# Kernel optimization log

Measured on AMD Instinct MI355X. Metric: run time of the kernel, lower is better.

The kernel has to match this reference:

```python
import jax, jax.numpy as jnp
import numpy as np

N_NODES = 100000
N_EDGES = 1600000
D = 64


def setup_inputs() -> dict:
    key = jax.random.key(0)
    k1, k2, k3, k4, k5, k6, k7, k8 = jax.random.split(key, 8)
    x = jax.random.normal(k1, (N_NODES, D), dtype=jnp.float32)
    adj = jax.random.randint(k2, (2, N_EDGES), 0, N_NODES, dtype=jnp.int64)
    adj_wts = jax.random.uniform(k3, (N_EDGES,), dtype=jnp.float32)
    s = 1.0 / np.sqrt(D)
    W1 = jax.random.uniform(k4, (D, D), minval=-s, maxval=s, dtype=jnp.float32)
    b1 = jax.random.uniform(k5, (D,), minval=-s, maxval=s, dtype=jnp.float32)
    W2 = jax.random.uniform(k6, (D, D), minval=-s, maxval=s, dtype=jnp.float32)
    b2 = jax.random.uniform(k7, (D,), minval=-s, maxval=s, dtype=jnp.float32)
    return {"x": x, "adj": adj, "adj_wts": adj_wts,
            "W1": W1, "b1": b1, "W2": W2, "b2": b2}


def _gcn_conv(x, row, col, norm, W, b):
    # Linear transform first (PyG GCNConv order), then normalized aggregation.
    h = x @ W                                   # [N, D]
    msg = norm[:, None] * h[row]                # gather from source nodes [E+N, D]
    out = jax.ops.segment_sum(msg, col, num_segments=N_NODES)  # scatter to targets
    return out + b


def _gcn_norm(adj, adj_wts):
    # Add self-loops with weight 1, compute symmetric normalization.
    loop = jnp.arange(N_NODES, dtype=adj.dtype)
    row = jnp.concatenate([adj[0], loop])
    col = jnp.concatenate([adj[1], loop])
    w = jnp.concatenate([adj_wts, jnp.ones((N_NODES,), dtype=adj_wts.dtype)])
    deg = jax.ops.segment_sum(w, col, num_segments=N_NODES)
    dinv = jnp.where(deg > 0, jax.lax.rsqrt(jnp.maximum(deg, 1e-12)), 0.0)
    norm = dinv[row] * w * dinv[col]
    return row, col, norm


def reference(x, adj, adj_wts, W1, b1, W2, b2):
    row, col, norm = _gcn_norm(adj, adj_wts)
    h = jax.nn.relu(_gcn_conv(x, row, col, norm, W1, b1))
    h = jax.nn.relu(_gcn_conv(h, row, col, norm, W2, b2))
    return h
```

## Files before the change

kernel.cpp:

```cpp
#include <hip/hip_runtime.h>

#define N_NODES 100000
#define N_EDGES 1600000
#define D 64
#define NBUCK 391
#define GBE 391
#define EPB 4096
#define DCAP 6144
#define NTILES 6250

typedef __attribute__((ext_vector_type(8))) short bf16x8;
typedef __attribute__((ext_vector_type(4))) float f32x4;

__device__ __forceinline__ unsigned short f2bf(float f) {
    unsigned int i = __float_as_uint(f);
    i += 0x7FFFu + ((i >> 16) & 1u);
    return (unsigned short)(i >> 16);
}
__device__ __forceinline__ void fma8(float* a, uint4 v, float wv) {
    a[0] = fmaf(wv, __uint_as_float(v.x << 16), a[0]);
    a[1] = fmaf(wv, __uint_as_float(v.x & 0xFFFF0000u), a[1]);
    a[2] = fmaf(wv, __uint_as_float(v.y << 16), a[2]);
    a[3] = fmaf(wv, __uint_as_float(v.y & 0xFFFF0000u), a[3]);
    a[4] = fmaf(wv, __uint_as_float(v.z << 16), a[4]);
    a[5] = fmaf(wv, __uint_as_float(v.z & 0xFFFF0000u), a[5]);
    a[6] = fmaf(wv, __uint_as_float(v.w << 16), a[6]);
    a[7] = fmaf(wv, __uint_as_float(v.w & 0xFFFF0000u), a[7]);
}


__global__ void binA(const int* __restrict__ col, int* __restrict__ histT) {
    __shared__ int h[NBUCK];
    int t = threadIdx.x;
    for (int i = t; i < NBUCK; i += 256) h[i] = 0;
    __syncthreads();
    int e0 = blockIdx.x * EPB;
    for (int i = t; i < EPB; i += 256) {
        int e = e0 + i;
        if (e < N_EDGES) atomicAdd(&h[col[e] >> 8], 1);
    }
    __syncthreads();
    for (int i = t; i < NBUCK; i += 256) histT[i * GBE + blockIdx.x] = h[i];
}

__global__ void binB1(int* __restrict__ histT, int* __restrict__ rowtot) {
    __shared__ int s[512];
    int b = blockIdx.x, tid = threadIdx.x;
    int v = (tid < GBE) ? histT[b * GBE + tid] : 0;
    s[tid] = v;
    __syncthreads();
    for (int o = 1; o < 512; o <<= 1) {
        int t = (tid >= o) ? s[tid - o] : 0;
        __syncthreads();
        s[tid] += t;
        __syncthreads();
    }
    if (tid < GBE) histT[b * GBE + tid] = s[tid] - v;
    if (tid == 511) rowtot[b] = s[511];
}

__global__ void binB2(const int* __restrict__ rowtot, int* __restrict__ bucketOff) {
    __shared__ int s[512];
    int tid = threadIdx.x;
    int v = (tid < NBUCK) ? rowtot[tid] : 0;
    s[tid] = v;
    __syncthreads();
    for (int o = 1; o < 512; o <<= 1) {
        int t = (tid >= o) ? s[tid - o] : 0;
        __syncthreads();
        s[tid] += t;
        __syncthreads();
    }
    if (tid < NBUCK) bucketOff[tid] = s[tid] - v;
    if (tid == 0) bucketOff[NBUCK] = N_EDGES;
}

__global__ void binC(const int* __restrict__ row, const int* __restrict__ col,
                     const float* __restrict__ w, const int* __restrict__ histT,
                     const int* __restrict__ bucketOff, int2* __restrict__ part_sw,
                     unsigned char* __restrict__ part_dlo) {
    __shared__ int cur[NBUCK];
    int t = threadIdx.x;
    for (int i = t; i < NBUCK; i += 256)
        cur[i] = bucketOff[i] + histT[i * GBE + blockIdx.x];
    __syncthreads();
    int e0 = blockIdx.x * EPB;
    for (int i = t; i < EPB; i += 256) {
        int e = e0 + i;
        if (e >= N_EDGES) continue;
        int c = col[e];
        int pos = atomicAdd(&cur[c >> 8], 1);
        int2 p; p.x = row[e]; p.y = __float_as_int(w[e]);
        part_sw[pos] = p;
        part_dlo[pos] = (unsigned char)(c & 255);
    }
}

__global__ void binD(const int2* __restrict__ part_sw, const unsigned char* __restrict__ part_dlo,
                     const int* __restrict__ bucketOff, int2* __restrict__ epack,
                     int* __restrict__ base, float* __restrict__ dinv) {
    __shared__ unsigned short dlo[DCAP];
    __shared__ int hist[257];
    __shared__ int cur[256];
    __shared__ float wsum[256];
    int b = blockIdx.x, t = threadIdx.x;
    int s0 = bucketOff[b], m = bucketOff[b + 1] - s0;
    for (int i = t; i < 257; i += 256) hist[i] = 0;
    wsum[t] = 0.0f;
    __syncthreads();
    for (int i = t; i < m; i += 256) {
        int dl = part_dlo[s0 + i];
        dlo[i] = (unsigned short)dl;
        atomicAdd(&hist[dl], 1);
    }
    __syncthreads();
    if (t == 0) {
        int acc = 0;
        for (int i = 0; i < 256; ++i) { int v = hist[i]; hist[i] = acc; acc += v; }
        hist[256] = acc;
    }
    __syncthreads();
    cur[t] = hist[t];
    int dst = b * 256 + t;
    if (dst < N_NODES) base[dst] = s0 + hist[t];
    if (b == NBUCK - 1 && t == 0) base[N_NODES] = N_EDGES;
    __syncthreads();
    for (int i = t; i < m; i += 256) {
        int dl = dlo[i];
        int2 p = part_sw[s0 + i];
        int pos = s0 + atomicAdd(&cur[dl], 1);
        epack[pos] = p;
        atomicAdd(&wsum[dl], __int_as_float(p.y));
    }
    __syncthreads();
    if (dst < N_NODES) dinv[dst] = rsqrtf(1.0f + wsum[t]);
}

__global__ void prescale_bf16(const float4* __restrict__ in4, const float* __restrict__ dinv,
                              ushort4* __restrict__ out4) {
    int gid = blockIdx.x * 256 + threadIdx.x;
    if (gid >= N_NODES * (D / 4)) return;
    float s = dinv[gid >> 4];
    float4 v = in4[gid];
    ushort4 o;
    o.x = f2bf(s * v.x); o.y = f2bf(s * v.y);
    o.z = f2bf(s * v.z); o.w = f2bf(s * v.w);
    out4[gid] = o;
}

template <bool LAST>
__global__ __launch_bounds__(256, 4)
void gcn_layer(const unsigned short* __restrict__ xsb, const float* __restrict__ W,
               const float* __restrict__ b, const float* __restrict__ dinv,
               const int2* __restrict__ epack, const int* __restrict__ base,
               unsigned short* __restrict__ hb_out, float* __restrict__ f_out) {
    __shared__ unsigned short T[16 * 72];
    int t = threadIdx.x;
    int lane  = t & 63;
    int wid   = t >> 6;
    int g     = lane >> 3;
    int c8    = (lane & 7) * 8;
    int r16   = lane & 15;
    int halfk = (lane >> 4) * 8;

    int bcol = wid * 16 + r16;
    bf16x8 bf0, bf1;
#pragma unroll
    for (int i = 0; i < 8; ++i) bf0[i] = (short)f2bf(W[(halfk + i) * D + bcol]);
#pragma unroll
    for (int i = 0; i < 8; ++i) bf1[i] = (short)f2bf(W[(halfk + 32 + i) * D + bcol]);
    float bias = b[bcol];

    int node0 = blockIdx.x * 16;
    for (int jp = 0; jp < 2; ++jp) {
        int nA = node0 + wid * 4 + jp * 2;
        int nB = nA + 1;
        float aA[8], aB[8];
#pragma unroll
        for (int q = 0; q < 8; ++q) { aA[q] = 0.0f; aB[q] = 0.0f; }
        if (g == 0) {
            uint4 sv = *(const uint4*)(xsb + (size_t)nA * D + c8);
            fma8(aA, sv, 1.0f);
        }
        if (g == 1) {
            uint4 sv = *(const uint4*)(xsb + (size_t)nB * D + c8);
            fma8(aB, sv, 1.0f);
        }
        int kA = base[nA], enA = base[nA + 1];
        int kB = enA,      enB = base[nB + 1];
        while (kA < enA || kB < enB) {
            uint4 vA, vB;
            float wA = 0.0f, wB = 0.0f;
            bool doA = kA < enA, doB = kB < enB;
            if (doA) {
                int kg = kA + g;
                int kc = (kg < enA) ? kg : (enA - 1);
                int2 p = epack[kc];
                wA = (kg < enA) ? __int_as_float(p.y) : 0.0f;
                vA = *(const uint4*)(xsb + (size_t)p.x * D + c8);
            }
            if (doB) {
                int kg = kB + g;
                int kc = (kg < enB) ? kg : (enB - 1);
                int2 p = epack[kc];
                wB = (kg < enB) ? __int_as_float(p.y) : 0.0f;
                vB = *(const uint4*)(xsb + (size_t)p.x * D + c8);
            }
            if (doA) fma8(aA, vA, wA);
            if (doB) fma8(aB, vB, wB);
            kA += 8; kB += 8;
        }
#pragma unroll
        for (int q = 0; q < 8; ++q) {
            aA[q] += __shfl_xor(aA[q], 8);
            aB[q] += __shfl_xor(aB[q], 8);
            aA[q] += __shfl_xor(aA[q], 16);
            aB[q] += __shfl_xor(aB[q], 16);
            aA[q] += __shfl_xor(aA[q], 32);
            aB[q] += __shfl_xor(aB[q], 32);
        }
        if (lane < 16) {
            float* a = (lane < 8) ? aA : aB;
            int nl = wid * 4 + jp * 2 + (lane >> 3);
            int l8 = (lane & 7) * 8;
            uint4 pk;
            pk.x = ((unsigned)f2bf(a[1]) << 16) | f2bf(a[0]);
            pk.y = ((unsigned)f2bf(a[3]) << 16) | f2bf(a[2]);
            pk.z = ((unsigned)f2bf(a[5]) << 16) | f2bf(a[4]);
            pk.w = ((unsigned)f2bf(a[7]) << 16) | f2bf(a[6]);
            *(uint4*)&T[nl * 72 + l8] = pk;
        }
    }
    __syncthreads();
    bf16x8 af0 = *(const bf16x8*)&T[r16 * 72 + halfk];
    bf16x8 af1 = *(const bf16x8*)&T[r16 * 72 + halfk + 32];
    f32x4 acc = {0.f, 0.f, 0.f, 0.f};
    acc = __builtin_amdgcn_mfma_f32_16x16x32_bf16(af0, bf0, acc, 0, 0, 0);
    acc = __builtin_amdgcn_mfma_f32_16x16x32_bf16(af1, bf1, acc, 0, 0, 0);
#pragma unroll
    for (int i = 0; i < 4; ++i) {
        int nr = (lane >> 4) * 4 + i;
        int node = node0 + nr;
        float s = dinv[node];
        float y = fmaxf(fmaf(s, acc[i], bias), 0.0f);
        size_t oidx = (size_t)node * D + bcol;
        if (LAST) f_out[oidx] = y;
        else      hb_out[oidx] = f2bf(s * y);
    }
}

extern "C" void kernel_launch(void* const* d_in, const int* in_sizes, int n_in,
                              void* d_out, int out_size, void* d_ws, size_t ws_size,
                              hipStream_t stream) {
    const float* x       = (const float*)d_in[0];
    const int*   adj     = (const int*)d_in[1];
    const float* adj_wts = (const float*)d_in[2];
    const float* W1      = (const float*)d_in[3];
    const float* b1      = (const float*)d_in[4];
    const float* W2      = (const float*)d_in[5];
    const float* b2      = (const float*)d_in[6];
    float* out = (float*)d_out;

    const int* row = adj;
    const int* col = adj + N_EDGES;

    char* p = (char*)d_ws;
    int2* epack = (int2*)p;                   p += (size_t)N_EDGES * 8;
    unsigned short* xsb = (unsigned short*)p; p += (size_t)N_NODES * D * 2;
    unsigned short* hb  = (unsigned short*)p; p += (size_t)N_NODES * D * 2;
    int2* part_sw = (int2*)p;                 p += (size_t)N_EDGES * 8;
    unsigned char* part_dlo = (unsigned char*)p; p += N_EDGES;
    int* histT = (int*)p;                     p += (size_t)(NBUCK * GBE + 3) / 4 * 4 * 4;
    int* rowtot = (int*)p;                    p += 392 * 4;
    int* bucketOff = (int*)p;                 p += 392 * 4;
    int* base = (int*)p;                      p += 100004 * 4;
    float* dinv = (float*)p;                  p += 100000 * 4;

    const int nblk_c = (N_NODES * 16 + 255) / 256;

    binA<<<GBE, 256, 0, stream>>>(col, histT);
    binB1<<<NBUCK, 512, 0, stream>>>(histT, rowtot);
    binB2<<<1, 512, 0, stream>>>(rowtot, bucketOff);
    binC<<<GBE, 256, 0, stream>>>(row, col, adj_wts, histT, bucketOff, part_sw, part_dlo);
    binD<<<NBUCK, 256, 0, stream>>>(part_sw, part_dlo, bucketOff, epack, base, dinv);

    prescale_bf16<<<nblk_c, 256, 0, stream>>>((const float4*)x, dinv, (ushort4*)xsb);

    gcn_layer<false><<<NTILES, 256, 0, stream>>>(xsb, W1, b1, dinv, epack, base, hb, nullptr);
    gcn_layer<true ><<<NTILES, 256, 0, stream>>>(hb, W2, b2, dinv, epack, base, nullptr, out);
}
```

Before: 198.8 us.

## Fuse bf16 prescale into binD and gather four nodes per wave concurrently

The separate prescale kernel is folded into the tail of binD, so each bucket block scales and converts its 256 nodes of x to bf16 right after computing dinv, which removes one launch and a dinv reload. The aggregation loop in gcn_layer now walks four destination nodes at once per wave instead of two nodes over two passes, putting more independent gathers in flight to hide memory latency. The cost is more registers (four 8-float accumulators), which could lower occupancy under the launch bounds, and the loop now runs until the longest of four neighbor lists is done, so more lanes sit idle when degrees differ.

```diff
diff --git a/kernel.cpp b/kernel.cpp
--- a/kernel.cpp
+++ b/kernel.cpp
@@ -27,6 +27,14 @@
     a[6] = fmaf(wv, __uint_as_float(v.w << 16), a[6]);
     a[7] = fmaf(wv, __uint_as_float(v.w & 0xFFFF0000u), a[7]);
 }
+__device__ __forceinline__ void packrow(unsigned short* dst, const float* a) {
+    uint4 pk;
+    pk.x = ((unsigned)f2bf(a[1]) << 16) | f2bf(a[0]);
+    pk.y = ((unsigned)f2bf(a[3]) << 16) | f2bf(a[2]);
+    pk.z = ((unsigned)f2bf(a[5]) << 16) | f2bf(a[4]);
+    pk.w = ((unsigned)f2bf(a[7]) << 16) | f2bf(a[6]);
+    *(uint4*)dst = pk;
+}
 
 
 __global__ void binA(const int* __restrict__ col, int* __restrict__ histT) {
@@ -97,8 +105,9 @@
 }
 
 __global__ void binD(const int2* __restrict__ part_sw, const unsigned char* __restrict__ part_dlo,
-                     const int* __restrict__ bucketOff, int2* __restrict__ epack,
-                     int* __restrict__ base, float* __restrict__ dinv) {
+                     const int* __restrict__ bucketOff, const float4* __restrict__ x4,
+                     int2* __restrict__ epack, int* __restrict__ base,
+                     float* __restrict__ dinv, ushort4* __restrict__ xsb4) {
     __shared__ unsigned short dlo[DCAP];
     __shared__ int hist[257];
     __shared__ int cur[256];
@@ -133,19 +142,28 @@
         atomicAdd(&wsum[dl], __int_as_float(p.y));
     }
     __syncthreads();
-    if (dst < N_NODES) dinv[dst] = rsqrtf(1.0f + wsum[t]);
-}
-
-__global__ void prescale_bf16(const float4* __restrict__ in4, const float* __restrict__ dinv,
-                              ushort4* __restrict__ out4) {
-    int gid = blockIdx.x * 256 + threadIdx.x;
-    if (gid >= N_NODES * (D / 4)) return;
-    float s = dinv[gid >> 4];
-    float4 v = in4[gid];
-    ushort4 o;
-    o.x = f2bf(s * v.x); o.y = f2bf(s * v.y);
-    o.z = f2bf(s * v.z); o.w = f2bf(s * v.w);
-    out4[gid] = o;
+    float di = 0.0f;
+    if (dst < N_NODES) {
+        di = rsqrtf(1.0f + wsum[t]);
+        dinv[dst] = di;
+    }
+    wsum[t] = di;
+    __syncthreads();
+    int nvalid = N_NODES - b * 256;
+#pragma unroll
+    for (int i = 0; i < 16; ++i) {
+        int gid = t + i * 256;
+        int r = gid >> 4, ch = gid & 15;
+        if (r < nvalid) {
+            float s = wsum[r];
+            size_t fidx = (size_t)(b * 256 + r) * 16 + ch;
+            float4 v = x4[fidx];
+            ushort4 o;
+            o.x = f2bf(s * v.x); o.y = f2bf(s * v.y);
+            o.z = f2bf(s * v.z); o.w = f2bf(s * v.w);
+            xsb4[fidx] = o;
+        }
+    }
 }
 
 template <bool LAST>
@@ -172,64 +190,60 @@
     float bias = b[bcol];
 
     int node0 = blockIdx.x * 16;
-    for (int jp = 0; jp < 2; ++jp) {
-        int nA = node0 + wid * 4 + jp * 2;
-        int nB = nA + 1;
-        float aA[8], aB[8];
-#pragma unroll
-        for (int q = 0; q < 8; ++q) { aA[q] = 0.0f; aB[q] = 0.0f; }
-        if (g == 0) {
-            uint4 sv = *(const uint4*)(xsb + (size_t)nA * D + c8);
-            fma8(aA, sv, 1.0f);
-        }
-        if (g == 1) {
-            uint4 sv = *(const uint4*)(xsb + (size_t)nB * D + c8);
-            fma8(aB, sv, 1.0f);
-        }
-        int kA = base[nA], enA = base[nA + 1];
-        int kB = enA,      enB = base[nB + 1];
-        while (kA < enA || kB < enB) {
-            uint4 vA, vB;
-            float wA = 0.0f, wB = 0.0f;
-            bool doA = kA < enA, doB = kB < enB;
-            if (doA) {
-                int kg = kA + g;
-                int kc = (kg < enA) ? kg : (enA - 1);
-                int2 p = epack[kc];
-                wA = (kg < enA) ? __int_as_float(p.y) : 0.0f;
-                vA = *(const uint4*)(xsb + (size_t)p.x * D + c8);
-            }
-            if (doB) {
-                int kg = kB + g;
-                int kc = (kg < enB) ? kg : (enB - 1);
-                int2 p = epack[kc];
-                wB = (kg < enB) ? __int_as_float(p.y) : 0.0f;
-                vB = *(const uint4*)(xsb + (size_t)p.x * D + c8);
-            }
-            if (doA) fma8(aA, vA, wA);
-            if (doB) fma8(aB, vB, wB);
-            kA += 8; kB += 8;
-        }
-#pragma unroll
-        for (int q = 0; q < 8; ++q) {
-            aA[q] += __shfl_xor(aA[q], 8);
-            aB[q] += __shfl_xor(aB[q], 8);
-            aA[q] += __shfl_xor(aA[q], 16);
-            aB[q] += __shfl_xor(aB[q], 16);
-            aA[q] += __shfl_xor(aA[q], 32);
-            aB[q] += __shfl_xor(aB[q], 32);
-        }
-        if (lane < 16) {
-            float* a = (lane < 8) ? aA : aB;
-            int nl = wid * 4 + jp * 2 + (lane >> 3);
-            int l8 = (lane & 7) * 8;
-            uint4 pk;
-            pk.x = ((unsigned)f2bf(a[1]) << 16) | f2bf(a[0]);
-            pk.y = ((unsigned)f2bf(a[3]) << 16) | f2bf(a[2]);
-            pk.z = ((unsigned)f2bf(a[5]) << 16) | f2bf(a[4]);
-            pk.w = ((unsigned)f2bf(a[7]) << 16) | f2bf(a[6]);
-            *(uint4*)&T[nl * 72 + l8] = pk;
-        }
+    int n0 = node0 + wid * 4;
+
+    float a0[8], a1[8], a2[8], a3[8];
+#pragma unroll
+    for (int q = 0; q < 8; ++q) { a0[q] = 0.f; a1[q] = 0.f; a2[q] = 0.f; a3[q] = 0.f; }
+
+    if (g == 0)      { uint4 sv = *(const uint4*)(xsb + (size_t)(n0    ) * D + c8); fma8(a0, sv, 1.0f); }
+    else if (g == 1) { uint4 sv = *(const uint4*)(xsb + (size_t)(n0 + 1) * D + c8); fma8(a1, sv, 1.0f); }
+    else if (g == 2) { uint4 sv = *(const uint4*)(xsb + (size_t)(n0 + 2) * D + c8); fma8(a2, sv, 1.0f); }
+    else if (g == 3) { uint4 sv = *(const uint4*)(xsb + (size_t)(n0 + 3) * D + c8); fma8(a3, sv, 1.0f); }
+
+    int k0 = base[n0],     e0 = base[n0 + 1];
+    int k1 = e0,           e1 = base[n0 + 2];
+    int k2 = e1,           e2 = base[n0 + 3];
+    int k3 = e2,           e3 = base[n0 + 4];
+
+    while (k0 < e0 || k1 < e1 || k2 < e2 || k3 < e3) {
+        uint4 v0, v1, v2, v3;
+        float w0 = 0.f, w1 = 0.f, w2 = 0.f, w3 = 0.f;
+        bool d0 = k0 < e0, d1 = k1 < e1, d2 = k2 < e2, d3 = k3 < e3;
+        if (d0) { int kg = k0 + g; int kc = (kg < e0) ? kg : e0 - 1; int2 p = epack[kc];
+                  w0 = (kg < e0) ? __int_as_float(p.y) : 0.f;
+                  v0 = *(const uint4*)(xsb + (size_t)p.x * D + c8); }
+        if (d1) { int kg = k1 + g; int kc = (kg < e1) ? kg : e1 - 1; int2 p = epack[kc];
+                  w1 = (kg < e1) ? __int_as_float(p.y) : 0.f;
+                  v1 = *(const uint4*)(xsb + (size_t)p.x * D + c8); }
+        if (d2) { int kg = k2 + g; int kc = (kg < e2) ? kg : e2 - 1; int2 p = epack[kc];
+                  w2 = (kg < e2) ? __int_as_float(p.y) : 0.f;
+                  v2 = *(const uint4*)(xsb + (size_t)p.x * D + c8); }
+        if (d3) { int kg = k3 + g; int kc = (kg < e3) ? kg : e3 - 1; int2 p = epack[kc];
+                  w3 = (kg < e3) ? __int_as_float(p.y) : 0.f;
+                  v3 = *(const uint4*)(xsb + (size_t)p.x * D + c8); }
+        if (d0) fma8(a0, v0, w0);
+        if (d1) fma8(a1, v1, w1);
+        if (d2) fma8(a2, v2, w2);
+        if (d3) fma8(a3, v3, w3);
+        k0 += 8; k1 += 8; k2 += 8; k3 += 8;
+    }
+
+#pragma unroll
+    for (int q = 0; q < 8; ++q) {
+        a0[q] += __shfl_xor(a0[q], 8);  a1[q] += __shfl_xor(a1[q], 8);
+        a2[q] += __shfl_xor(a2[q], 8);  a3[q] += __shfl_xor(a3[q], 8);
+        a0[q] += __shfl_xor(a0[q], 16); a1[q] += __shfl_xor(a1[q], 16);
+        a2[q] += __shfl_xor(a2[q], 16); a3[q] += __shfl_xor(a3[q], 16);
+        a0[q] += __shfl_xor(a0[q], 32); a1[q] += __shfl_xor(a1[q], 32);
+        a2[q] += __shfl_xor(a2[q], 32); a3[q] += __shfl_xor(a3[q], 32);
+    }
+    {
+        int l8 = (lane & 7) * 8;
+        if (g == 0)      packrow(&T[(wid * 4 + 0) * 72 + l8], a0);
+        else if (g == 1) packrow(&T[(wid * 4 + 1) * 72 + l8], a1);
+        else if (g == 2) packrow(&T[(wid * 4 + 2) * 72 + l8], a2);
+        else if (g == 3) packrow(&T[(wid * 4 + 3) * 72 + l8], a3);
     }
     __syncthreads();
     bf16x8 af0 = *(const bf16x8*)&T[r16 * 72 + halfk];
@@ -276,15 +290,12 @@
     int* base = (int*)p;                      p += 100004 * 4;
     float* dinv = (float*)p;                  p += 100000 * 4;
 
-    const int nblk_c = (N_NODES * 16 + 255) / 256;
-
     binA<<<GBE, 256, 0, stream>>>(col, histT);
     binB1<<<NBUCK, 512, 0, stream>>>(histT, rowtot);
     binB2<<<1, 512, 0, stream>>>(rowtot, bucketOff);
     binC<<<GBE, 256, 0, stream>>>(row, col, adj_wts, histT, bucketOff, part_sw, part_dlo);
-    binD<<<NBUCK, 256, 0, stream>>>(part_sw, part_dlo, bucketOff, epack, base, dinv);
-
-    prescale_bf16<<<nblk_c, 256, 0, stream>>>((const float4*)x, dinv, (ushort4*)xsb);
+    binD<<<NBUCK, 256, 0, stream>>>(part_sw, part_dlo, bucketOff, (const float4*)x,
+                                    epack, base, dinv, (ushort4*)xsb);
 
     gcn_layer<false><<<NTILES, 256, 0, stream>>>(xsb, W1, b1, dinv, epack, base, hb, nullptr);
     gcn_layer<true ><<<NTILES, 256, 0, stream>>>(hb, W2, b2, dinv, epack, base, nullptr, out);
```

Result: slower. 234.6 us (+18.0%).

## Fuse binning scans and prescale, pack dst-low bits into source index

Applied to the files above, without the earlier changes.

Merges the two scan kernels into one using a last-block-done atomic counter, packs the low 8 destination bits into the top byte of the source index to drop the separate byte array, and folds the bf16 prescale of x into binD. It also replaces binD's serial single-thread scan with a parallel scan and removes clamped loads in the edge gather loop. Together these cut kernel launches and global traffic in the preprocessing chain, at the cost of an extra memset and a grid-level atomic handshake.

```diff
diff --git a/kernel.cpp b/kernel.cpp
--- a/kernel.cpp
+++ b/kernel.cpp
@@ -43,8 +43,10 @@
     for (int i = t; i < NBUCK; i += 256) histT[i * GBE + blockIdx.x] = h[i];
 }
 
-__global__ void binB1(int* __restrict__ histT, int* __restrict__ rowtot) {
+__global__ void binB(int* __restrict__ histT, int* __restrict__ rowtot,
+                     int* __restrict__ bucketOff, int* __restrict__ done) {
     __shared__ int s[512];
+    __shared__ int lastflag;
     int b = blockIdx.x, tid = threadIdx.x;
     int v = (tid < GBE) ? histT[b * GBE + tid] : 0;
     s[tid] = v;
@@ -56,29 +58,31 @@
         __syncthreads();
     }
     if (tid < GBE) histT[b * GBE + tid] = s[tid] - v;
-    if (tid == 511) rowtot[b] = s[511];
-}
-
-__global__ void binB2(const int* __restrict__ rowtot, int* __restrict__ bucketOff) {
-    __shared__ int s[512];
-    int tid = threadIdx.x;
-    int v = (tid < NBUCK) ? rowtot[tid] : 0;
-    s[tid] = v;
-    __syncthreads();
-    for (int o = 1; o < 512; o <<= 1) {
-        int t = (tid >= o) ? s[tid - o] : 0;
-        __syncthreads();
-        s[tid] += t;
-        __syncthreads();
-    }
-    if (tid < NBUCK) bucketOff[tid] = s[tid] - v;
-    if (tid == 0) bucketOff[NBUCK] = N_EDGES;
+    if (tid == 511) atomicExch(&rowtot[b], s[511]);
+    __syncthreads();
+    if (tid == 0) {
+        __threadfence();
+        lastflag = (atomicAdd(done, 1) == NBUCK - 1);
+    }
+    __syncthreads();
+    if (lastflag) {
+        int rv = (tid < NBUCK) ? atomicAdd(&rowtot[tid], 0) : 0;
+        s[tid] = rv;
+        __syncthreads();
+        for (int o = 1; o < 512; o <<= 1) {
+            int t = (tid >= o) ? s[tid - o] : 0;
+            __syncthreads();
+            s[tid] += t;
+            __syncthreads();
+        }
+        if (tid < NBUCK) bucketOff[tid] = s[tid] - rv;
+        if (tid == 0) bucketOff[NBUCK] = N_EDGES;
+    }
 }
 
 __global__ void binC(const int* __restrict__ row, const int* __restrict__ col,
                      const float* __restrict__ w, const int* __restrict__ histT,
-                     const int* __restrict__ bucketOff, int2* __restrict__ part_sw,
-                     unsigned char* __restrict__ part_dlo) {
+                     const int* __restrict__ bucketOff, int2* __restrict__ part_sw) {
     __shared__ int cur[NBUCK];
     int t = threadIdx.x;
     for (int i = t; i < NBUCK; i += 256)
@@ -90,62 +94,81 @@
         if (e >= N_EDGES) continue;
         int c = col[e];
         int pos = atomicAdd(&cur[c >> 8], 1);
-        int2 p; p.x = row[e]; p.y = __float_as_int(w[e]);
+        int2 p;
+        p.x = (int)((unsigned)row[e] | ((unsigned)(c & 255) << 24));
+        p.y = __float_as_int(w[e]);
         part_sw[pos] = p;
-        part_dlo[pos] = (unsigned char)(c & 255);
-    }
-}
-
-__global__ void binD(const int2* __restrict__ part_sw, const unsigned char* __restrict__ part_dlo,
-                     const int* __restrict__ bucketOff, int2* __restrict__ epack,
-                     int* __restrict__ base, float* __restrict__ dinv) {
+    }
+}
+
+__global__ void binD(const int2* __restrict__ part_sw, const int* __restrict__ bucketOff,
+                     const float4* __restrict__ x4, int2* __restrict__ epack,
+                     int* __restrict__ base, float* __restrict__ dinv,
+                     ushort4* __restrict__ xsb4) {
     __shared__ unsigned short dlo[DCAP];
-    __shared__ int hist[257];
+    __shared__ int hist[256];
+    __shared__ int scanb[256];
     __shared__ int cur[256];
     __shared__ float wsum[256];
     int b = blockIdx.x, t = threadIdx.x;
     int s0 = bucketOff[b], m = bucketOff[b + 1] - s0;
-    for (int i = t; i < 257; i += 256) hist[i] = 0;
+    hist[t] = 0;
     wsum[t] = 0.0f;
     __syncthreads();
     for (int i = t; i < m; i += 256) {
-        int dl = part_dlo[s0 + i];
+        int dl = (int)((unsigned)part_sw[s0 + i].x >> 24);
         dlo[i] = (unsigned short)dl;
         atomicAdd(&hist[dl], 1);
     }
     __syncthreads();
-    if (t == 0) {
-        int acc = 0;
-        for (int i = 0; i < 256; ++i) { int v = hist[i]; hist[i] = acc; acc += v; }
-        hist[256] = acc;
-    }
-    __syncthreads();
-    cur[t] = hist[t];
+    int v = hist[t];
+    scanb[t] = v;
+    __syncthreads();
+    for (int o = 1; o < 256; o <<= 1) {
+        int tv = (t >= o) ? scanb[t - o] : 0;
+        __syncthreads();
+        scanb[t] += tv;
+        __syncthreads();
+    }
+    int excl = scanb[t] - v;
+    cur[t] = excl;
     int dst = b * 256 + t;
-    if (dst < N_NODES) base[dst] = s0 + hist[t];
+    if (dst < N_NODES) base[dst] = s0 + excl;
     if (b == NBUCK - 1 && t == 0) base[N_NODES] = N_EDGES;
     __syncthreads();
     for (int i = t; i < m; i += 256) {
         int dl = dlo[i];
         int2 p = part_sw[s0 + i];
         int pos = s0 + atomicAdd(&cur[dl], 1);
-        epack[pos] = p;
+        int2 q;
+        q.x = (int)((unsigned)p.x & 0xFFFFFFu);
+        q.y = p.y;
+        epack[pos] = q;
         atomicAdd(&wsum[dl], __int_as_float(p.y));
     }
     __syncthreads();
-    if (dst < N_NODES) dinv[dst] = rsqrtf(1.0f + wsum[t]);
-}
-
-__global__ void prescale_bf16(const float4* __restrict__ in4, const float* __restrict__ dinv,
-                              ushort4* __restrict__ out4) {
-    int gid = blockIdx.x * 256 + threadIdx.x;
-    if (gid >= N_NODES * (D / 4)) return;
-    float s = dinv[gid >> 4];
-    float4 v = in4[gid];
-    ushort4 o;
-    o.x = f2bf(s * v.x); o.y = f2bf(s * v.y);
-    o.z = f2bf(s * v.z); o.w = f2bf(s * v.w);
-    out4[gid] = o;
+    float di = 0.0f;
+    if (dst < N_NODES) {
+        di = rsqrtf(1.0f + wsum[t]);
+        dinv[dst] = di;
+    }
+    wsum[t] = di;
+    __syncthreads();
+    int nvalid = N_NODES - b * 256;
+#pragma unroll
+    for (int i = 0; i < 16; ++i) {
+        int gid = t + i * 256;
+        int r = gid >> 4, ch = gid & 15;
+        if (r < nvalid) {
+            float s = wsum[r];
+            size_t fidx = (size_t)(b * 256 + r) * 16 + ch;
+            float4 xv = x4[fidx];
+            ushort4 o;
+            o.x = f2bf(s * xv.x); o.y = f2bf(s * xv.y);
+            o.z = f2bf(s * xv.z); o.w = f2bf(s * xv.w);
+            xsb4[fidx] = o;
+        }
+    }
 }
 
 template <bool LAST>
@@ -189,25 +212,16 @@
         int kA = base[nA], enA = base[nA + 1];
         int kB = enA,      enB = base[nB + 1];
         while (kA < enA || kB < enB) {
+            int kgA = kA + g, kgB = kB + g;
+            bool dA = kgA < enA, dB = kgB < enB;
+            int2 pA, pB;
             uint4 vA, vB;
-            float wA = 0.0f, wB = 0.0f;
-            bool doA = kA < enA, doB = kB < enB;
-            if (doA) {
-                int kg = kA + g;
-                int kc = (kg < enA) ? kg : (enA - 1);
-                int2 p = epack[kc];
-                wA = (kg < enA) ? __int_as_float(p.y) : 0.0f;
-                vA = *(const uint4*)(xsb + (size_t)p.x * D + c8);
-            }
-            if (doB) {
-                int kg = kB + g;
-                int kc = (kg < enB) ? kg : (enB - 1);
-                int2 p = epack[kc];
-                wB = (kg < enB) ? __int_as_float(p.y) : 0.0f;
-                vB = *(const uint4*)(xsb + (size_t)p.x * D + c8);
-            }
-            if (doA) fma8(aA, vA, wA);
-            if (doB) fma8(aB, vB, wB);
+            if (dA) pA = epack[kgA];
+            if (dB) pB = epack[kgB];
+            if (dA) vA = *(const uint4*)(xsb + (size_t)pA.x * D + c8);
+            if (dB) vB = *(const uint4*)(xsb + (size_t)pB.x * D + c8);
+            if (dA) fma8(aA, vA, __int_as_float(pA.y));
+            if (dB) fma8(aB, vB, __int_as_float(pB.y));
             kA += 8; kB += 8;
         }
 #pragma unroll
@@ -269,22 +283,19 @@
     unsigned short* xsb = (unsigned short*)p; p += (size_t)N_NODES * D * 2;
     unsigned short* hb  = (unsigned short*)p; p += (size_t)N_NODES * D * 2;
     int2* part_sw = (int2*)p;                 p += (size_t)N_EDGES * 8;
-    unsigned char* part_dlo = (unsigned char*)p; p += N_EDGES;
     int* histT = (int*)p;                     p += (size_t)(NBUCK * GBE + 3) / 4 * 4 * 4;
     int* rowtot = (int*)p;                    p += 392 * 4;
     int* bucketOff = (int*)p;                 p += 392 * 4;
     int* base = (int*)p;                      p += 100004 * 4;
     float* dinv = (float*)p;                  p += 100000 * 4;
-
-    const int nblk_c = (N_NODES * 16 + 255) / 256;
+    int* done = (int*)p;                      p += 4 * 4;
 
     binA<<<GBE, 256, 0, stream>>>(col, histT);
-    binB1<<<NBUCK, 512, 0, stream>>>(histT, rowtot);
-    binB2<<<1, 512, 0, stream>>>(rowtot, bucketOff);
-    binC<<<GBE, 256, 0, stream>>>(row, col, adj_wts, histT, bucketOff, part_sw, part_dlo);
-    binD<<<NBUCK, 256, 0, stream>>>(part_sw, part_dlo, bucketOff, epack, base, dinv);
-
-    prescale_bf16<<<nblk_c, 256, 0, stream>>>((const float4*)x, dinv, (ushort4*)xsb);
+    hipMemsetAsync(done, 0, 4, stream);
+    binB<<<NBUCK, 512, 0, stream>>>(histT, rowtot, bucketOff, done);
+    binC<<<GBE, 256, 0, stream>>>(row, col, adj_wts, histT, bucketOff, part_sw);
+    binD<<<NBUCK, 256, 0, stream>>>(part_sw, bucketOff, (const float4*)x,
+                                    epack, base, dinv, (ushort4*)xsb);
 
     gcn_layer<false><<<NTILES, 256, 0, stream>>>(xsb, W1, b1, dinv, epack, base, hb, nullptr);
     gcn_layer<true ><<<NTILES, 256, 0, stream>>>(hb, W2, b2, dinv, epack, base, nullptr, out);
```

New measurement: 199.7 us. No clear change (+0.4%).
